# Kernel optimization log

Measured on AMD Instinct MI355X. Metric: run time of the kernel, lower is better.

## Reference

```python
import jax, jax.numpy as jnp
import numpy as np

B, N, K, C, L = 8, 16384, 128, 128, 4
IN_DIM, NDIMS, FC_DIM, OUT_DIM = 3, 2, 128, 1


def setup_inputs() -> dict:
    key = jax.random.key(0)
    ks = jax.random.split(key, 16)
    scale = 1.0 / (C * C)
    return {
        "x": jax.random.normal(ks[0], (B, N, IN_DIM), jnp.float32),
        "nodes": jax.random.uniform(ks[1], (B, N, NDIMS), jnp.float32),
        "node_mask": jnp.ones((B, N, 1), jnp.float32),
        "node_weights": jax.random.uniform(ks[2], (B, N, 1), jnp.float32) / N,
        "modes": jax.random.normal(ks[3], (K, NDIMS), jnp.float32) * 3.0,
        "fc0_w": jax.random.normal(ks[4], (IN_DIM, C), jnp.float32) * 0.1,
        "fc0_b": jax.random.normal(ks[5], (C,), jnp.float32) * 0.1,
        "wc": scale * jax.random.uniform(ks[6], (L, C, C, K), jnp.float32),
        "ws_": scale * jax.random.uniform(ks[7], (L, C, C, K), jnp.float32),
        "w0": scale * jax.random.uniform(ks[8], (L, C, C, 1), jnp.float32),
        "conv_w": jax.random.normal(ks[9], (L, C, C), jnp.float32) * (1.0 / np.sqrt(C)),
        "conv_b": jax.random.normal(ks[10], (L, C), jnp.float32) * 0.1,
        "fc1_w": jax.random.normal(ks[11], (C, FC_DIM), jnp.float32) * (1.0 / np.sqrt(C)),
        "fc1_b": jax.random.normal(ks[12], (FC_DIM,), jnp.float32) * 0.1,
        "fc2_w": jax.random.normal(ks[13], (FC_DIM, OUT_DIM), jnp.float32) * (1.0 / np.sqrt(FC_DIM)),
        "fc2_b": jax.random.normal(ks[14], (OUT_DIM,), jnp.float32) * 0.1,
    }


def _gelu(x):
    # torch F.gelu default = exact erf gelu
    return jax.nn.gelu(x, approximate=False)


def reference(x, nodes, node_mask, node_weights, modes, fc0_w, fc0_b,
              wc, ws_, w0, conv_w, conv_b, fc1_w, fc1_b, fc2_w, fc2_b):
    # Fourier bases: [B, N, K]
    temp = jnp.einsum("bxd,kd->bxk", nodes, modes)
    bases_c = jnp.cos(temp) * node_mask
    bases_s = jnp.sin(temp) * node_mask
    bases_0 = node_mask  # [B, N, 1]
    wbases_c = bases_c * node_weights
    wbases_s = bases_s * node_weights
    wbases_0 = bases_0 * node_weights

    h = x @ fc0_w + fc0_b            # [B, N, C]
    h = jnp.transpose(h, (0, 2, 1))  # [B, C, N]

    nlayers = wc.shape[0]
    for i in range(nlayers):
        # forward projection onto modes: [B, C, K]
        x_c_hat = jnp.einsum("bix,bxk->bik", h, wbases_c)
        x_s_hat = -jnp.einsum("bix,bxk->bik", h, wbases_s)
        x_0_hat = jnp.einsum("bix,bxk->bik", h, wbases_0)
        # complex weight mixing
        f_c_hat = jnp.einsum("bik,iok->bok", x_c_hat, wc[i]) - jnp.einsum("bik,iok->bok", x_s_hat, ws_[i])
        f_s_hat = jnp.einsum("bik,iok->bok", x_s_hat, wc[i]) + jnp.einsum("bik,iok->bok", x_c_hat, ws_[i])
        f_0_hat = jnp.einsum("bik,iok->bok", x_0_hat, w0[i])
        # inverse projection back to nodes: [B, C, N]
        x1 = (jnp.einsum("bok,bxk->box", f_0_hat, bases_0)
              + 2.0 * jnp.einsum("bok,bxk->box", f_c_hat, bases_c)
              - 2.0 * jnp.einsum("bok,bxk->box", f_s_hat, bases_s))
        # pointwise Conv1d kernel-size-1
        x2 = jnp.einsum("oi,bix->box", conv_w[i], h) + conv_b[i][None, :, None]
        h = x1 + x2
        if i != nlayers - 1:
            h = _gelu(h)

    h = jnp.transpose(h, (0, 2, 1))  # [B, N, C]
    h = _gelu(h @ fc1_w + fc1_b)
    h = h @ fc2_w + fc2_b            # [B, N, out_dim]
    return h * node_mask
```

## Files before the change

### kernel.cpp

```cpp
#include <hip/hip_runtime.h>

using u16 = unsigned short;
typedef short bf8 __attribute__((ext_vector_type(8)));
typedef float f4 __attribute__((ext_vector_type(4)));

constexpr int Bb = 8;
constexpr int Nn = 16384;
constexpr int Kk = 128;
constexpr int Cc = 128;
constexpr int Ll = 4;
constexpr int SPLIT = 32;

__device__ __forceinline__ float b2f(u16 u) {
    union { unsigned int i; float f; } v; v.i = ((unsigned int)u) << 16; return v.f;
}
__device__ __forceinline__ u16 f2b(float f) {
    union { float f; unsigned int i; } v; v.f = f;
    unsigned int i = v.i;
    return (u16)((i + 0x7fffu + ((i >> 16) & 1u)) >> 16);
}
__device__ __forceinline__ float gelu_f(float x) {
    return 0.5f * x * (1.0f + erff(x * 0.70710678118654752f));
}

__global__ void detect_kernel(const unsigned int* __restrict__ maskw, int* __restrict__ flag) {
    if (threadIdx.x == 0 && blockIdx.x == 0)
        *flag = ((maskw[0] & 0xFFFFu) != 0u) ? 1 : 0;
}

struct SegTable {
    const void* src[16];
    u16* dst[16];
    int count[16];
};

__global__ __launch_bounds__(256) void convert_kernel(SegTable t, const int* __restrict__ flag) {
    const int f = *flag;
    const int stride = gridDim.x * 256;
    for (int seg = 0; seg < 16; ++seg) {
        const int cnt = t.count[seg];
        const void* s = t.src[seg];
        u16* d = t.dst[seg];
        for (int i = blockIdx.x * 256 + threadIdx.x; i < cnt; i += stride) {
            d[i] = f ? ((const u16*)s)[i] : f2b(((const float*)s)[i]);
        }
    }
}

__global__ __launch_bounds__(256) void bases_nk_kernel(
    const u16* __restrict__ nodes, const u16* __restrict__ modes,
    const u16* __restrict__ mask, u16* __restrict__ bigB) {
    int t = threadIdx.x;
    int nl = t >> 2, kp = t & 3;
    int n = blockIdx.x * 64 + nl, b = blockIdx.y;
    float nx = b2f(nodes[((size_t)(b * Nn + n)) * 2]);
    float ny = b2f(nodes[((size_t)(b * Nn + n)) * 2 + 1]);
    float mk = b2f(mask[b * Nn + n]);
    u16 cb[32] __attribute__((aligned(16)));
    u16 sb[32] __attribute__((aligned(16)));
    #pragma unroll
    for (int j = 0; j < 32; j++) {
        int k = kp * 32 + j;
        float m0 = b2f(modes[k * 2]), m1 = b2f(modes[k * 2 + 1]);
        float tt = nx * m0 + ny * m1;
        cb[j] = f2b(__cosf(tt) * mk);
        sb[j] = f2b(__sinf(tt) * mk);
    }
    u16* row = bigB + ((size_t)b * Nn + n) * 256;
    #pragma unroll
    for (int i = 0; i < 4; i++) {
        *(uint4*)(row + kp * 32 + i * 8)       = *(const uint4*)(cb + i * 8);
        *(uint4*)(row + 128 + kp * 32 + i * 8) = *(const uint4*)(sb + i * 8);
    }
}

__global__ __launch_bounds__(256) void fc0_nk_kernel(
    const u16* __restrict__ x, const u16* __restrict__ fc0_w,
    const u16* __restrict__ fc0_b, const u16* __restrict__ wn,
    u16* __restrict__ hA, u16* __restrict__ hw_cn) {
    int t = threadIdx.x;
    int nl = t >> 2, cp = t & 3;
    int n = blockIdx.x * 64 + nl, b = blockIdx.y;
    const u16* xp = x + ((size_t)(b * Nn + n)) * 3;
    float x0v = b2f(xp[0]), x1v = b2f(xp[1]), x2v = b2f(xp[2]);
    float wv = b2f(wn[b * Nn + n]);
    u16 hb[32] __attribute__((aligned(16)));
    #pragma unroll
    for (int j = 0; j < 32; j++) {
        int c = cp * 32 + j;
        float acc = b2f(fc0_b[c]);
        acc += x0v * b2f(fc0_w[0 * Cc + c]);
        acc += x1v * b2f(fc0_w[1 * Cc + c]);
        acc += x2v * b2f(fc0_w[2 * Cc + c]);
        hb[j] = f2b(acc);
        hw_cn[((size_t)(b * Cc + c)) * Nn + n] = f2b(acc * wv);
    }
    u16* row = hA + ((size_t)b * Nn + n) * 128 + cp * 32;
    #pragma unroll
    for (int i = 0; i < 4; i++) *(uint4*)(row + i * 8) = *(const uint4*)(hb + i * 8);
}

__global__ __launch_bounds__(256) void transpose_w(
    const void* __restrict__ wcraw, const void* __restrict__ wsraw,
    const u16* __restrict__ w0n,
    u16* __restrict__ wcT, u16* __restrict__ wsT, u16* __restrict__ w0T,
    const int* __restrict__ flag) {
    __shared__ u16 tile[128][136];
    int o = blockIdx.x, l = blockIdx.y, t = threadIdx.x;
    const int f = *flag;
    if (o == 128) {
        int i = t >> 1, oh = (t & 1) * 64;
        #pragma unroll
        for (int j = 0; j < 64; j += 8)
            *(uint4*)&tile[i][oh + j] = *(const uint4*)(w0n + ((size_t)(l * 128 + i)) * 128 + oh + j);
        __syncthreads();
        int o2 = t >> 1, ih = (t & 1) * 64;
        u16 buf[64] __attribute__((aligned(16)));
        #pragma unroll
        for (int j = 0; j < 64; j++) buf[j] = tile[ih + j][o2];
        #pragma unroll
        for (int j = 0; j < 64; j += 8)
            *(uint4*)(w0T + ((size_t)(l * 128 + o2)) * 128 + ih + j) = *(const uint4*)(buf + j);
        return;
    }
    for (int wsel = 0; wsel < 2; wsel++) {
        if (wsel) __syncthreads();
        const void* raw = wsel ? wsraw : wcraw;
        u16* dst = wsel ? wsT : wcT;
        int i = t >> 1, kh = (t & 1) * 64;
        size_t base = (((size_t)(l * 128 + i)) * 128 + o) * 128 + kh;
        if (f) {
            #pragma unroll
            for (int j = 0; j < 64; j += 8)
                *(uint4*)&tile[i][kh + j] = *(const uint4*)((const u16*)raw + base + j);
        } else {
            #pragma unroll
            for (int j = 0; j < 64; j += 4) {
                float4 v = *(const float4*)((const float*)raw + base + j);
                u16 o4[4] __attribute__((aligned(8))) = { f2b(v.x), f2b(v.y), f2b(v.z), f2b(v.w) };
                *(unsigned long long*)&tile[i][kh + j] = *(const unsigned long long*)o4;
            }
        }
        __syncthreads();
        int k = t >> 1, ih = (t & 1) * 64;
        u16 buf[64] __attribute__((aligned(16)));
        #pragma unroll
        for (int j = 0; j < 64; j++) buf[j] = tile[ih + j][k];
        #pragma unroll
        for (int j = 0; j < 64; j += 8)
            *(uint4*)(dst + (((size_t)(l * 128 + k)) * 128 + o) * 128 + ih + j) = *(const uint4*)(buf + j);
    }
}

__global__ __launch_bounds__(256) void x0_kernel(
    const u16* __restrict__ hw, const u16* __restrict__ mask,
    float* __restrict__ x0, u16* __restrict__ x0b) {
    int c = blockIdx.x, b = blockIdx.y;
    const u16* row = hw + ((size_t)(b * Cc + c)) * Nn;
    const u16* mrow = mask + (size_t)b * Nn;
    float acc = 0.f;
    for (int n = threadIdx.x; n < Nn; n += 256) acc += b2f(row[n]) * b2f(mrow[n]);
    __shared__ float red[4];
    for (int off = 32; off; off >>= 1) acc += __shfl_down(acc, off, 64);
    if ((threadIdx.x & 63) == 0) red[threadIdx.x >> 6] = acc;
    __syncthreads();
    if (threadIdx.x == 0) {
        float v = red[0] + red[1] + red[2] + red[3];
        x0[b * Cc + c] = v;
        x0b[b * Cc + c] = f2b(v);
    }
}

__global__ __launch_bounds__(256) void proj_mfma(
    const u16* __restrict__ hw, const u16* __restrict__ nodes,
    const u16* __restrict__ modes, const u16* __restrict__ mask,
    u16* __restrict__ pxc, u16* __restrict__ pps) {
    int s = blockIdx.x, kh = blockIdx.y, b = blockIdx.z;
    int w = threadIdx.x >> 6, lane = threadIdx.x & 63;
    int lo = lane & 15, q = lane >> 4;
    int n0 = s * 512;
    int kmode = kh * 32 + (w & 1) * 16 + lo;
    int ch = w >> 1;
    float m0 = b2f(modes[kmode * 2]), m1 = b2f(modes[kmode * 2 + 1]);
    const u16* ap[4];
    #pragma unroll
    for (int ct = 0; ct < 4; ct++)
        ap[ct] = hw + ((size_t)(b * Cc) + ch * 64 + ct * 16 + lo) * Nn + n0 + q * 8;
    const u16* np = nodes + ((size_t)(b * Nn) + n0 + q * 8) * 2;
    const u16* mp = mask + (size_t)b * Nn + n0 + q * 8;
    f4 aC[4] = {}, aS[4] = {};
    for (int js = 0; js < 16; js++) {
        int off = js * 32;
        uint4 nq0 = *(const uint4*)(np + off * 2);
        uint4 nq1 = *(const uint4*)(np + off * 2 + 8);
        uint4 mq  = *(const uint4*)(mp + off);
        float xs[8], ys[8], mk[8];
        xs[0] = b2f(nq0.x & 0xffffu); ys[0] = b2f(nq0.x >> 16);
        xs[1] = b2f(nq0.y & 0xffffu); ys[1] = b2f(nq0.y >> 16);
        xs[2] = b2f(nq0.z & 0xffffu); ys[2] = b2f(nq0.z >> 16);
        xs[3] = b2f(nq0.w & 0xffffu); ys[3] = b2f(nq0.w >> 16);
        xs[4] = b2f(nq1.x & 0xffffu); ys[4] = b2f(nq1.x >> 16);
        xs[5] = b2f(nq1.y & 0xffffu); ys[5] = b2f(nq1.y >> 16);
        xs[6] = b2f(nq1.z & 0xffffu); ys[6] = b2f(nq1.z >> 16);
        xs[7] = b2f(nq1.w & 0xffffu); ys[7] = b2f(nq1.w >> 16);
        mk[0] = b2f(mq.x & 0xffffu);  mk[1] = b2f(mq.x >> 16);
        mk[2] = b2f(mq.y & 0xffffu);  mk[3] = b2f(mq.y >> 16);
        mk[4] = b2f(mq.z & 0xffffu);  mk[5] = b2f(mq.z >> 16);
        mk[6] = b2f(mq.w & 0xffffu);  mk[7] = b2f(mq.w >> 16);
        u16 cf[8] __attribute__((aligned(16)));
        u16 sf[8] __attribute__((aligned(16)));
        #pragma unroll
        for (int j = 0; j < 8; j++) {
            float tt = xs[j] * m0 + ys[j] * m1;
            cf[j] = f2b(__cosf(tt) * mk[j]);
            sf[j] = f2b(__sinf(tt) * mk[j]);
        }
        bf8 cv = *(const bf8*)cf;
        bf8 sv = *(const bf8*)sf;
        #pragma unroll
        for (int ct = 0; ct < 4; ct++) {
            bf8 av = *(const bf8*)(ap[ct] + off);
            aC[ct] = __builtin_amdgcn_mfma_f32_16x16x32_bf16(av, cv, aC[ct], 0, 0, 0);
            aS[ct] = __builtin_amdgcn_mfma_f32_16x16x32_bf16(av, sv, aS[ct], 0, 0, 0);
        }
    }
    size_t base = ((size_t)(b * SPLIT + s)) * 16384 + (size_t)kmode * 128;
    #pragma unroll
    for (int ct = 0; ct < 4; ct++) {
        int c0 = ch * 64 + ct * 16 + q * 4;
        u16 pc[4] __attribute__((aligned(8)));
        u16 pssv[4] __attribute__((aligned(8)));
        #pragma unroll
        for (int r = 0; r < 4; r++) { pc[r] = f2b(aC[ct][r]); pssv[r] = f2b(aS[ct][r]); }
        *(uint2*)&pxc[base + c0] = *(const uint2*)pc;
        *(uint2*)&pps[base + c0] = *(const uint2*)pssv;
    }
}

__global__ __launch_bounds__(256) void reduce_kernel(
    const u16* __restrict__ pxc, const u16* __restrict__ pps,
    u16* __restrict__ xcT, u16* __restrict__ psT) {
    int g = blockIdx.x * 256 + threadIdx.x;
    int b = g >> 14, r = g & 16383;
    const u16* p1 = pxc + ((size_t)b * SPLIT) * 16384 + r;
    const u16* p2 = pps + ((size_t)b * SPLIT) * 16384 + r;
    float a1 = 0.f, a2 = 0.f;
    #pragma unroll
    for (int s2 = 0; s2 < SPLIT; s2++) {
        a1 += b2f(p1[(size_t)s2 * 16384]);
        a2 += b2f(p2[(size_t)s2 * 16384]);
    }
    xcT[g] = f2b(a1); psT[g] = f2b(a2);
}

__global__ __launch_bounds__(256) void mix_mfma(
    const u16* __restrict__ xcT, const u16* __restrict__ psT,
    const u16* __restrict__ wcT, const u16* __restrict__ wsT,
    const u16* __restrict__ w0T, const u16* __restrict__ x0b,
    u16* __restrict__ Ablk, float* __restrict__ f0p, int l) {
    int kb = blockIdx.x;
    int w = threadIdx.x >> 6, lane = threadIdx.x & 63;
    int lo = lane & 15, q = lane >> 4;
    if (kb == 128) {
        const u16* Arow = x0b + (lo & 7) * 128 + q * 8;
        f4 acc[2] = {};
        #pragma unroll
        for (int step = 0; step < 4; step++) {
            bf8 av = *(const bf8*)(Arow + step * 32);
            #pragma unroll
            for (int nt = 0; nt < 2; nt++) {
                int o = w * 32 + nt * 16 + lo;
                bf8 bv = *(const bf8*)(w0T + ((size_t)(l * 128 + o)) * 128 + q * 8 + step * 32);
                acc[nt] = __builtin_amdgcn_mfma_f32_16x16x32_bf16(av, bv, acc[nt], 0, 0, 0);
            }
        }
        if (q < 2) {
            #pragma unroll
            for (int nt = 0; nt < 2; nt++)
                #pragma unroll
                for (int r = 0; r < 4; r++) {
                    int bb = q * 4 + r, o = w * 32 + nt * 16 + lo;
                    f0p[bb * 128 + o] = acc[nt][r];
                }
        }
        return;
    }
    int k = kb;
    const u16* Arow = (lo < 8)
        ? xcT + ((size_t)(lo * 128 + k)) * 128 + q * 8
        : psT + ((size_t)((lo - 8) * 128 + k)) * 128 + q * 8;
    const u16* wc_l = wcT + ((size_t)(l * 128 + k)) * (128 * 128);
    const u16* ws_l = wsT + ((size_t)(l * 128 + k)) * (128 * 128);
    f4 accC[2] = {}, accS[2] = {};
    #pragma unroll
    for (int step = 0; step < 4; step++) {
        bf8 av = *(const bf8*)(Arow + step * 32);
        #pragma unroll
        for (int nt = 0; nt < 2; nt++) {
            int o = w * 32 + nt * 16 + lo;
            bf8 bc = *(const bf8*)(wc_l + (size_t)o * 128 + q * 8 + step * 32);
            bf8 bs = *(const bf8*)(ws_l + (size_t)o * 128 + q * 8 + step * 32);
            accC[nt] = __builtin_amdgcn_mfma_f32_16x16x32_bf16(av, bc, accC[nt], 0, 0, 0);
            accS[nt] = __builtin_amdgcn_mfma_f32_16x16x32_bf16(av, bs, accS[nt], 0, 0, 0);
        }
    }
    #pragma unroll
    for (int nt = 0; nt < 2; nt++)
        #pragma unroll
        for (int r = 0; r < 4; r++) {
            float uc = accC[nt][r], us = accS[nt][r];
            float ucp = __shfl_xor(uc, 32, 64);
            float usp = __shfl_xor(us, 32, 64);
            if (q < 2) {
                int bb = q * 4 + r, o = w * 32 + nt * 16 + lo;
                float fcv = uc + usp;
                float fsv = us - ucp;
                Ablk[(((size_t)(bb * 12 + (k >> 5))) * 128 + o) * 32 + (k & 31)] = f2b(2.f * fcv);
                Ablk[(((size_t)(bb * 12 + 4 + (k >> 5))) * 128 + o) * 32 + (k & 31)] = f2b(-2.f * fsv);
            }
        }
}

__global__ __launch_bounds__(256) void conv_fill(
    const u16* __restrict__ conv_w, u16* __restrict__ Ablk, int l) {
    int ks2 = blockIdx.x, b = blockIdx.y, t = threadIdx.x;
    int o = t >> 1, half = t & 1;
    const u16* src = conv_w + ((size_t)(l * 128 + o)) * 128 + ks2 * 32 + half * 16;
    u16* dst = Ablk + (((size_t)(b * 12 + 8 + ks2)) * 128 + o) * 32 + half * 16;
    *(uint4*)dst = *(const uint4*)src;
    *(uint4*)(dst + 8) = *(const uint4*)(src + 8);
}

__global__ __launch_bounds__(256) void buildA1_blk(
    const u16* __restrict__ fc1_w, u16* __restrict__ Ablk1) {
    int ks = blockIdx.x, t = threadIdx.x;
    int o = t >> 1, half = t & 1;
    u16 ov[16] __attribute__((aligned(16)));
    #pragma unroll
    for (int j = 0; j < 16; j++) {
        int kk = ks * 32 + half * 16 + j;
        ov[j] = fc1_w[kk * 128 + o];
    }
    u16* dst = Ablk1 + ((size_t)ks * 128 + o) * 32 + half * 16;
    *(uint4*)dst = *(const uint4*)ov;
    *(uint4*)(dst + 8) = *(const uint4*)(ov + 8);
}

template <int EPI, int NKS>
__global__ __launch_bounds__(256) void combine_mfma(
    const u16* __restrict__ Ablk, long astr,
    const u16* __restrict__ bigB, u16* __restrict__ h,
    u16* __restrict__ hw_cn,
    const float* __restrict__ f0p, const u16* __restrict__ bias,
    const u16* __restrict__ mask, const u16* __restrict__ wn,
    const u16* __restrict__ fc2w, float* __restrict__ psum) {
    __shared__ u16 lds[20480];
    int b = blockIdx.y;
    int nb = blockIdx.x * 128;
    int t = threadIdx.x;
    int w = t >> 6, lane = t & 63;
    int lo = lane & 15, q = lane >> 4;
    int wo = (w & 1) * 64, wn2 = (w >> 1) * 64;

    u16* abuf[2] = { lds, lds + 5120 };
    u16* bbuf[2] = { lds + 10240, lds + 15360 };

    const u16* Ab = Ablk + (size_t)b * astr;
    int so = t >> 1, sh = t & 1;
    size_t brow = (size_t)b * Nn + nb + so;
    const u16* bigRow = bigB + brow * 256 + sh * 16;
    const u16* hRow   = h    + brow * 128 + sh * 16;

    uint4 ra0, ra1, rb0, rb1;
    auto loadGlob = [&](int ksn, uint4& a0, uint4& a1, uint4& b0, uint4& b1) {
        const u16* asrc = Ab + (size_t)ksn * 4096 + so * 32 + sh * 16;
        a0 = *(const uint4*)asrc;
        a1 = *(const uint4*)(asrc + 8);
        const u16* bsrc;
        if (EPI == 2) bsrc = hRow + ksn * 32;
        else bsrc = (ksn < 8) ? (bigRow + ksn * 32) : (hRow + (ksn - 8) * 32);
        b0 = *(const uint4*)bsrc;
        b1 = *(const uint4*)(bsrc + 8);
    };
    auto stash = [&](int pb, uint4 a0, uint4 a1, uint4 b0, uint4 b1) {
        u16* ad = abuf[pb] + so * 40 + sh * 16;
        *(uint4*)ad = a0; *(uint4*)(ad + 8) = a1;
        u16* bd = bbuf[pb] + so * 40 + sh * 16;
        *(uint4*)bd = b0; *(uint4*)(bd + 8) = b1;
    };

    loadGlob(0, ra0, ra1, rb0, rb1);
    stash(0, ra0, ra1, rb0, rb1);
    f4 acc[4][4] = {};
    #pragma unroll
    for (int ks = 0; ks < NKS; ks++) {
        __syncthreads();
        if (ks + 1 < NKS) loadGlob(ks + 1, ra0, ra1, rb0, rb1);
        int pb = ks & 1;
        bf8 avf[4], bvf[4];
        #pragma unroll
        for (int ot = 0; ot < 4; ot++)
            avf[ot] = *(const bf8*)(abuf[pb] + (wo + ot * 16 + lo) * 40 + q * 8);
        #pragma unroll
        for (int nt = 0; nt < 4; nt++)
            bvf[nt] = *(const bf8*)(bbuf[pb] + (wn2 + nt * 16 + lo) * 40 + q * 8);
        #pragma unroll
        for (int ot = 0; ot < 4; ot++)
            #pragma unroll
            for (int nt = 0; nt < 4; nt++)
                acc[ot][nt] = __builtin_amdgcn_mfma_f32_16x16x32_bf16(avf[ot], bvf[nt], acc[ot][nt], 0, 0, 0);
        if (ks + 1 < NKS) stash(1 - pb, ra0, ra1, rb0, rb1);
    }
    __syncthreads();

    if (EPI == 2) {
        #pragma unroll
        for (int nt = 0; nt < 4; nt++) {
            int n = nb + wn2 + nt * 16 + lo;
            float s = 0.f;
            #pragma unroll
            for (int ot = 0; ot < 4; ot++)
                #pragma unroll
                for (int r = 0; r < 4; r++) {
                    int o = wo + ot * 16 + q * 4 + r;
                    float v = acc[ot][nt][r] + b2f(bias[o]);
                    v = gelu_f(v);
                    s += b2f(fc2w[o]) * v;
                }
            s += __shfl_xor(s, 16, 64);
            s += __shfl_xor(s, 32, 64);
            if (q == 0)
                psum[(size_t)(w & 1) * (Bb * Nn) + (size_t)b * Nn + n] = s;
        }
    } else {
        u16* tile = lds + w * 4352;
        #pragma unroll
        for (int nt = 0; nt < 4; nt++) {
            int n = nb + wn2 + nt * 16 + lo;
            float mv = b2f(mask[(size_t)b * Nn + n]);
            #pragma unroll
            for (int ot = 0; ot < 4; ot++) {
                u16 hv[4] __attribute__((aligned(8)));
                #pragma unroll
                for (int r = 0; r < 4; r++) {
                    int o = wo + ot * 16 + q * 4 + r;
                    float v = acc[ot][nt][r] + b2f(bias[o]) + f0p[b * Cc + o] * mv;
                    if (EPI == 0) v = gelu_f(v);
                    hv[r] = f2b(v);
                }
                *(uint2*)&tile[(nt * 16 + lo) * 68 + ot * 16 + q * 4] = *(const uint2*)hv;
            }
        }
        __syncthreads();
        #pragma unroll
        for (int it = 0; it < 8; it++) {
            int row = it * 8 + (lane >> 3), seg = lane & 7;
            uint4 v4 = *(const uint4*)&tile[row * 68 + seg * 8];
            *(uint4*)&h[((size_t)b * Nn + nb + wn2 + row) * 128 + wo + seg * 8] = v4;
        }
        if (EPI == 0) {
            int c = wo + lane;
            const u16* wnp = wn + (size_t)b * Nn + nb + wn2;
            u16* dstp = hw_cn + ((size_t)(b * Cc) + c) * Nn + nb + wn2;
            #pragma unroll
            for (int i = 0; i < 8; i++) {
                u16 hv8[8] __attribute__((aligned(16)));
                #pragma unroll
                for (int j2 = 0; j2 < 8; j2++) {
                    int nl2 = i * 8 + j2;
                    hv8[j2] = f2b(b2f(tile[nl2 * 68 + lane]) * b2f(wnp[nl2]));
                }
                *(uint4*)(dstp + i * 8) = *(const uint4*)hv8;
            }
        }
    }
}

__global__ __launch_bounds__(256) void fc2_final(
    const float* __restrict__ psum, const u16* __restrict__ fc2b,
    const u16* __restrict__ mask, void* __restrict__ out, const int* __restrict__ flag) {
    int g = blockIdx.x * 256 + threadIdx.x;
    float s = psum[g] + psum[(size_t)Bb * Nn + g] + b2f(fc2b[0]);
    s *= b2f(mask[g]);
    if (*flag) ((u16*)out)[g] = f2b(s);
    else       ((float*)out)[g] = s;
}

extern "C" void kernel_launch(void* const* d_in, const int* in_sizes, int n_in,
                              void* d_out, int out_size, void* d_ws, size_t ws_size,
                              hipStream_t stream) {
    char* p = (char*)d_ws;
    auto alloc = [&](size_t bytes) { void* r = (void*)p; p += (bytes + 255) & ~(size_t)255; return r; };

    int* flag = (int*)alloc(256);

    SegTable tab;
    u16* nin[16];
    for (int i = 0; i < 16; i++) {
        tab.src[i] = d_in[i];
        if (i == 7 || i == 8) {
            nin[i] = (u16*)flag;
            tab.dst[i] = nin[i];
            tab.count[i] = 0;
        } else {
            int cnt = in_sizes[i];
            nin[i] = (u16*)alloc((size_t)cnt * 2);
            tab.dst[i] = nin[i];
            tab.count[i] = cnt;
        }
    }
    const u16* x      = nin[0];
    const u16* nodes  = nin[1];
    const u16* mask   = nin[2];
    const u16* wn     = nin[3];
    const u16* modes  = nin[4];
    const u16* fc0_w  = nin[5];
    const u16* fc0_b  = nin[6];
    const u16* w0n    = nin[9];
    const u16* conv_w = nin[10];
    const u16* conv_b = nin[11];
    const u16* fc1_w  = nin[12];
    const u16* fc1_b  = nin[13];
    const u16* fc2_w  = nin[14];
    const u16* fc2_b  = nin[15];

    u16* bigB   = (u16*)alloc((size_t)Bb * Nn * 256 * 2);
    u16* hA     = (u16*)alloc((size_t)Bb * Nn * 128 * 2);
    u16* hw_cn  = (u16*)alloc((size_t)Bb * Cc * Nn * 2);
    u16* pxc    = (u16*)alloc((size_t)Bb * SPLIT * Cc * Kk * 2);
    u16* pps    = (u16*)alloc((size_t)Bb * SPLIT * Cc * Kk * 2);
    u16* wcT    = (u16*)alloc((size_t)Ll * Kk * Cc * Cc * 2);
    u16* wsT    = (u16*)alloc((size_t)Ll * Kk * Cc * Cc * 2);
    u16* w0T    = (u16*)alloc((size_t)Ll * Cc * Cc * 2);
    u16* xcT    = (u16*)alloc((size_t)Bb * Kk * Cc * 2);
    u16* psT    = (u16*)alloc((size_t)Bb * Kk * Cc * 2);
    float* x0f  = (float*)alloc((size_t)Bb * Cc * 4);
    u16* x0b    = (u16*)alloc((size_t)Bb * Cc * 2);
    float* f0f  = (float*)alloc((size_t)Bb * Cc * 4);
    u16* Ablk   = (u16*)alloc((size_t)Bb * 12 * 128 * 32 * 2);
    u16* Ablk1  = (u16*)alloc((size_t)4 * 128 * 32 * 2);
    float* psum = (float*)alloc((size_t)2 * Bb * Nn * 4);

    const long ASTR = 12L * 128 * 32;

    detect_kernel<<<1, 64, 0, stream>>>((const unsigned int*)d_in[2], flag);
    convert_kernel<<<512, 256, 0, stream>>>(tab, flag);

    transpose_w<<<dim3(129, Ll), 256, 0, stream>>>(d_in[7], d_in[8], w0n, wcT, wsT, w0T, flag);
    bases_nk_kernel<<<dim3(Nn / 64, Bb), 256, 0, stream>>>(nodes, modes, mask, bigB);
    fc0_nk_kernel<<<dim3(Nn / 64, Bb), 256, 0, stream>>>(x, fc0_w, fc0_b, wn, hA, hw_cn);

    for (int l = 0; l < Ll; l++) {
        x0_kernel<<<dim3(Cc, Bb), 256, 0, stream>>>(hw_cn, mask, x0f, x0b);
        proj_mfma<<<dim3(SPLIT, 4, Bb), 256, 0, stream>>>(hw_cn, nodes, modes, mask, pxc, pps);
        reduce_kernel<<<dim3((Bb * Cc * Kk) / 256), 256, 0, stream>>>(pxc, pps, xcT, psT);
        conv_fill<<<dim3(4, Bb), 256, 0, stream>>>(conv_w, Ablk, l);
        mix_mfma<<<dim3(129), 256, 0, stream>>>(xcT, psT, wcT, wsT, w0T, x0b, Ablk, f0f, l);
        if (l < Ll - 1) {
            combine_mfma<0, 12><<<dim3(Nn / 128, Bb), 256, 0, stream>>>(
                Ablk, ASTR, bigB, hA, hw_cn, f0f, conv_b + l * Cc, mask, wn, fc2_w, psum);
        } else {
            combine_mfma<1, 12><<<dim3(Nn / 128, Bb), 256, 0, stream>>>(
                Ablk, ASTR, bigB, hA, hw_cn, f0f, conv_b + l * Cc, mask, wn, fc2_w, psum);
        }
    }

    buildA1_blk<<<dim3(4), 256, 0, stream>>>(fc1_w, Ablk1);
    combine_mfma<2, 4><<<dim3(Nn / 128, Bb), 256, 0, stream>>>(
        Ablk1, 0L, bigB, hA, hw_cn, f0f, fc1_b, mask, wn, fc2_w, psum);
    fc2_final<<<dim3((Bb * Nn) / 256), 256, 0, stream>>>(psum, fc2_b, mask, d_out, flag);
}
```

Measured before the change: 705.9 us.

## Load MFMA fragments directly from global memory, dropping LDS staging in combine kernel

The combine_mfma kernel no longer stages A and B tiles through double-buffered shared memory with block-wide barriers. Each wave now loads its own bf16 MFMA fragments straight from global memory into registers and prefetches the next k-step into a second register set. This removes the LDS round trip and the __syncthreads per k-step. In exchange, A tiles are read redundantly by multiple waves, the global loads are narrower per lane and less coalesced, and register pressure rises, which could hurt latency hiding.

```diff
diff --git a/kernel.cpp b/kernel.cpp
--- a/kernel.cpp
+++ b/kernel.cpp
@@ -354,7 +354,7 @@
     const float* __restrict__ f0p, const u16* __restrict__ bias,
     const u16* __restrict__ mask, const u16* __restrict__ wn,
     const u16* __restrict__ fc2w, float* __restrict__ psum) {
-    __shared__ u16 lds[20480];
+    __shared__ u16 lds[17408];
     int b = blockIdx.y;
     int nb = blockIdx.x * 128;
     int t = threadIdx.x;
@@ -362,56 +362,47 @@
     int lo = lane & 15, q = lane >> 4;
     int wo = (w & 1) * 64, wn2 = (w >> 1) * 64;
 
-    u16* abuf[2] = { lds, lds + 5120 };
-    u16* bbuf[2] = { lds + 10240, lds + 15360 };
-
     const u16* Ab = Ablk + (size_t)b * astr;
-    int so = t >> 1, sh = t & 1;
-    size_t brow = (size_t)b * Nn + nb + so;
-    const u16* bigRow = bigB + brow * 256 + sh * 16;
-    const u16* hRow   = h    + brow * 128 + sh * 16;
-
-    uint4 ra0, ra1, rb0, rb1;
-    auto loadGlob = [&](int ksn, uint4& a0, uint4& a1, uint4& b0, uint4& b1) {
-        const u16* asrc = Ab + (size_t)ksn * 4096 + so * 32 + sh * 16;
-        a0 = *(const uint4*)asrc;
-        a1 = *(const uint4*)(asrc + 8);
-        const u16* bsrc;
-        if (EPI == 2) bsrc = hRow + ksn * 32;
-        else bsrc = (ksn < 8) ? (bigRow + ksn * 32) : (hRow + (ksn - 8) * 32);
-        b0 = *(const uint4*)bsrc;
-        b1 = *(const uint4*)(bsrc + 8);
+    const u16* aBase = Ab + (size_t)(wo + lo) * 32 + q * 8;
+    const u16* bB[4];
+    const u16* bH[4];
+    #pragma unroll
+    for (int nt = 0; nt < 4; nt++) {
+        size_t row = (size_t)b * Nn + nb + wn2 + nt * 16 + lo;
+        bB[nt] = bigB + row * 256 + q * 8;
+        bH[nt] = h + row * 128 + q * 8;
+    }
+
+    auto loadFrag = [&](int ks, bf8* av, bf8* bv) {
+        #pragma unroll
+        for (int ot = 0; ot < 4; ot++)
+            av[ot] = *(const bf8*)(aBase + (size_t)ks * 4096 + ot * 512);
+        #pragma unroll
+        for (int nt = 0; nt < 4; nt++) {
+            const u16* src;
+            if (EPI == 2)      src = bH[nt] + ks * 32;
+            else if (ks < 8)   src = bB[nt] + ks * 32;
+            else               src = bH[nt] + (ks - 8) * 32;
+            bv[nt] = *(const bf8*)src;
+        }
     };
-    auto stash = [&](int pb, uint4 a0, uint4 a1, uint4 b0, uint4 b1) {
-        u16* ad = abuf[pb] + so * 40 + sh * 16;
-        *(uint4*)ad = a0; *(uint4*)(ad + 8) = a1;
-        u16* bd = bbuf[pb] + so * 40 + sh * 16;
-        *(uint4*)bd = b0; *(uint4*)(bd + 8) = b1;
-    };
-
-    loadGlob(0, ra0, ra1, rb0, rb1);
-    stash(0, ra0, ra1, rb0, rb1);
+
     f4 acc[4][4] = {};
+    bf8 ca[4], cbv[4], na[4], nbv[4];
+    loadFrag(0, ca, cbv);
     #pragma unroll
     for (int ks = 0; ks < NKS; ks++) {
-        __syncthreads();
-        if (ks + 1 < NKS) loadGlob(ks + 1, ra0, ra1, rb0, rb1);
-        int pb = ks & 1;
-        bf8 avf[4], bvf[4];
+        if (ks + 1 < NKS) loadFrag(ks + 1, na, nbv);
         #pragma unroll
         for (int ot = 0; ot < 4; ot++)
-            avf[ot] = *(const bf8*)(abuf[pb] + (wo + ot * 16 + lo) * 40 + q * 8);
-        #pragma unroll
-        for (int nt = 0; nt < 4; nt++)
-            bvf[nt] = *(const bf8*)(bbuf[pb] + (wn2 + nt * 16 + lo) * 40 + q * 8);
-        #pragma unroll
-        for (int ot = 0; ot < 4; ot++)
             #pragma unroll
             for (int nt = 0; nt < 4; nt++)
-                acc[ot][nt] = __builtin_amdgcn_mfma_f32_16x16x32_bf16(avf[ot], bvf[nt], acc[ot][nt], 0, 0, 0);
-        if (ks + 1 < NKS) stash(1 - pb, ra0, ra1, rb0, rb1);
-    }
-    __syncthreads();
+                acc[ot][nt] = __builtin_amdgcn_mfma_f32_16x16x32_bf16(ca[ot], cbv[nt], acc[ot][nt], 0, 0, 0);
+        if (ks + 1 < NKS) {
+            #pragma unroll
+            for (int i = 0; i < 4; i++) { ca[i] = na[i]; cbv[i] = nbv[i]; }
+        }
+    }
 
     if (EPI == 2) {
         #pragma unroll
```

Result: slower. 767.3 us (+8.7%).
